# Performance work log

Hardware: AMD Instinct MI355X
Metric: run time of the kernel (lower is better)

The kernel has to match this reference:

```python
import jax, jax.numpy as jnp
import numpy as np

NH = 8        # num_heads
KS = 64       # key_size
C_IN = 256
C_OUT = 3 * NH * KS   # 1536
GROUPS = 3 * NH       # 24
EPS = 1e-5
H = W = 64


def setup_inputs() -> dict:
    key = jax.random.key(0)
    k1, k2 = jax.random.split(key)
    x = jax.random.normal(k1, (1, C_IN, H, W), dtype=jnp.float32)
    conv_w = jax.random.normal(k2, (C_OUT, C_IN, 1, 1), dtype=jnp.float32) * 0.05
    gn_w = jnp.ones((C_OUT,), dtype=jnp.float32)
    gn_b = jnp.zeros((C_OUT,), dtype=jnp.float32)
    return {"x": x, "conv_w": conv_w, "gn_w": gn_w, "gn_b": gn_b}


def reference(x, conv_w, gn_w, gn_b):
    B, _, h, w = x.shape
    # 1x1 conv (normalize=True -> no bias): per-pixel GEMM over channels
    attn = jnp.einsum('bchw,oc->bohw', x, conv_w[:, :, 0, 0])  # [B, 1536, H, W]
    # GroupNorm: 24 groups of KS channels, normalized over (KS, H, W)
    g = attn.reshape(B, GROUPS, -1)
    mean = g.mean(axis=-1, keepdims=True)
    var = g.var(axis=-1, keepdims=True)
    g = (g - mean) * jax.lax.rsqrt(var + EPS)
    attn = g.reshape(B, C_OUT, h, w) * gn_w[None, :, None, None] + gn_b[None, :, None, None]
    # split into key, query, value (in that order, per chunk(3, dim=2))
    attn = attn.reshape(B, NH, 3 * KS, h * w)
    key_, query, value = jnp.split(attn, 3, axis=2)   # each [B, NH, KS, HW]
    # saliency = q^T @ k / sqrt(KS) -> [B, NH, HW, HW]
    saliency = jnp.einsum('bnkq,bnkl->bnql', query, key_) / jnp.sqrt(jnp.float32(KS))
    mask = jax.nn.softmax(saliency, axis=-1)
    # out = v @ mask^T -> [B, NH, KS, HW]
    out = jnp.einsum('bnkl,bnql->bnkq', value, mask)
    return out.reshape(B, NH * KS, h, w)
```

## Files before the change

kernel.cpp:

```cpp
#include <hip/hip_runtime.h>

typedef __bf16 bf16;
typedef __bf16 bf16x8 __attribute__((ext_vector_type(8)));
typedef __bf16 bf16x4 __attribute__((ext_vector_type(4)));
typedef float f32x4 __attribute__((ext_vector_type(4)));
typedef float f32x16 __attribute__((ext_vector_type(16)));


#define QF 0.18033688011112042f
#define EXPF(x) __builtin_amdgcn_exp2f(x)

union U4 { bf16x4 v; unsigned u[2]; };
union U8 { bf16x8 v; unsigned u[4]; };

__global__ void k_misc(const float* __restrict__ x, const float* __restrict__ w,
                       bf16* __restrict__ xT, bf16* __restrict__ wb, float* __restrict__ cs) {
    int b = blockIdx.x;
    if (b < 256) {
        __shared__ float ld[64][65];
        int cb = (b & 3) * 64;
        int pb = (b >> 2) * 64;
        int tp = (threadIdx.x & 15) * 4;
        int tc = threadIdx.x >> 4;
#pragma unroll
        for (int pass = 0; pass < 4; pass++) {
            int c = tc + pass * 16;
            float4 f = *(const float4*)(x + (cb + c) * 4096 + pb + tp);
            ld[tp][c] = f.x; ld[tp + 1][c] = f.y; ld[tp + 2][c] = f.z; ld[tp + 3][c] = f.w;
        }
        __syncthreads();
        int px = threadIdx.x >> 3;
        int co = (threadIdx.x & 7) * 8;
#pragma unroll
        for (int pass = 0; pass < 2; pass++) {
            int p2 = px + pass * 32;
            bf16x8 o;
#pragma unroll
            for (int j = 0; j < 8; j++) o[j] = (bf16)ld[p2][co + j];
            *(bf16x8*)(xT + (pb + p2) * 256 + cb + co) = o;
        }
    } else if (b < 640) {
        int idx = ((b - 256) * 256 + threadIdx.x) * 4;
        float4 f = *(const float4*)(w + idx);
        bf16x4 o;
        o[0] = (bf16)f.x; o[1] = (bf16)f.y; o[2] = (bf16)f.z; o[3] = (bf16)f.w;
        *(bf16x4*)(wb + idx) = o;
    } else {
#pragma unroll
        for (int i = 0; i < 12; i++) cs[i * 256 + threadIdx.x] = 0.f;
    }
}

__global__ __launch_bounds__(256) void k_conv(const bf16* __restrict__ Wb,
                                              const bf16* __restrict__ xT,
                                              bf16* __restrict__ qkvT,
                                              float* __restrict__ cs) {
    __shared__ __attribute__((aligned(16))) bf16 xs[64 * 72];
    __shared__ __attribute__((aligned(16))) bf16 ws2[64 * 72];
    int wid = threadIdx.x >> 6, lane = threadIdx.x & 63;
    int quad = lane >> 4, l15 = lane & 15;
    int g  = blockIdx.x % 24;
    int pb = (blockIdx.x / 24) * 64;
    int h = g / 3, sec = g % 3;
    int ob = g * 64;

    int srow = threadIdx.x >> 2;
    int scol = (threadIdx.x & 3) * 16;

    f32x4 acc[4];
#pragma unroll
    for (int c = 0; c < 4; c++) acc[c] = (f32x4){0.f, 0.f, 0.f, 0.f};

    bf16x8 fx0 = *(const bf16x8*)(xT + (pb + srow) * 256 + scol);
    bf16x8 fx1 = *(const bf16x8*)(xT + (pb + srow) * 256 + scol + 8);
    bf16x8 fw0 = *(const bf16x8*)(Wb + (ob + srow) * 256 + scol);
    bf16x8 fw1 = *(const bf16x8*)(Wb + (ob + srow) * 256 + scol + 8);

    for (int c4 = 0; c4 < 4; c4++) {
        __syncthreads();
        *(bf16x8*)(xs  + srow * 72 + scol)     = fx0;
        *(bf16x8*)(xs  + srow * 72 + scol + 8) = fx1;
        *(bf16x8*)(ws2 + srow * 72 + scol)     = fw0;
        *(bf16x8*)(ws2 + srow * 72 + scol + 8) = fw1;
        __syncthreads();

        if (c4 < 3) {
            int co = (c4 + 1) * 64;
            fx0 = *(const bf16x8*)(xT + (pb + srow) * 256 + co + scol);
            fx1 = *(const bf16x8*)(xT + (pb + srow) * 256 + co + scol + 8);
            fw0 = *(const bf16x8*)(Wb + (ob + srow) * 256 + co + scol);
            fw1 = *(const bf16x8*)(Wb + (ob + srow) * 256 + co + scol + 8);
        }

#pragma unroll
        for (int k2 = 0; k2 < 2; k2++) {
            bf16x8 a = *(const bf16x8*)(ws2 + (wid * 16 + l15) * 72 + k2 * 32 + quad * 8);
#pragma unroll
            for (int c = 0; c < 4; c++) {
                bf16x8 b = *(const bf16x8*)(xs + (c * 16 + l15) * 72 + k2 * 32 + quad * 8);
                acc[c] = __builtin_amdgcn_mfma_f32_16x16x32_bf16(a, b, acc[c], 0, 0, 0);
            }
        }
    }

    int ch0 = wid * 16 + quad * 4;
#pragma unroll
    for (int r = 0; r < 4; r++) {
        float sp  = acc[0][r] + acc[1][r] + acc[2][r] + acc[3][r];
        float ssp = acc[0][r] * acc[0][r] + acc[1][r] * acc[1][r]
                  + acc[2][r] * acc[2][r] + acc[3][r] * acc[3][r];
#pragma unroll
        for (int m = 1; m < 16; m <<= 1) {
            sp  += __shfl_xor(sp,  m, 64);
            ssp += __shfl_xor(ssp, m, 64);
        }
        if (l15 == 0) {
            atomicAdd(cs + (ob + ch0 + r) * 2,     sp);
            atomicAdd(cs + (ob + ch0 + r) * 2 + 1, ssp);
        }
    }

    __syncthreads();
    bf16* tile = xs;
    if (sec == 2) {
#pragma unroll
        for (int c = 0; c < 4; c++)
#pragma unroll
            for (int r = 0; r < 4; r++)
                tile[(ch0 + r) * 72 + c * 16 + l15] = (bf16)acc[c][r];
    } else {
#pragma unroll
        for (int c = 0; c < 4; c++) {
            bf16x4 o;
#pragma unroll
            for (int r = 0; r < 4; r++) o[r] = (bf16)acc[c][r];
            *(bf16x4*)(&tile[(c * 16 + l15) * 72 + ch0]) = o;
        }
    }
    __syncthreads();
    bf16* base = qkvT + h * 786432;
    int t = threadIdx.x;
    if (sec == 2) {
        bf16* V = base + 524288;
#pragma unroll
        for (int it = 0; it < 2; it++) {
            int e = it * 256 + t; int ch = e >> 3; int pxo = (e & 7) * 8;
            *(bf16x8*)(V + ch * 4096 + pb + pxo) = *(const bf16x8*)(&tile[ch * 72 + pxo]);
        }
    } else {
        bf16* dst = base + (sec == 0 ? 262144 : 0);
#pragma unroll
        for (int it = 0; it < 2; it++) {
            int e = it * 256 + t; int px = e >> 3; int cho = (e & 7) * 8;
            *(bf16x8*)(dst + (pb + px) * 64 + cho) = *(const bf16x8*)(&tile[px * 72 + cho]);
        }
    }
}

#define PF_BLOCK(S, PFA, PFB)                                                   \
    {                                                                           \
        float p0 = EXPF(S[0]),  p1 = EXPF(S[1]),  p2 = EXPF(S[2]),  p3 = EXPF(S[3]);   \
        float p4 = EXPF(S[4]),  p5 = EXPF(S[5]),  p6 = EXPF(S[6]),  p7 = EXPF(S[7]);   \
        float p8 = EXPF(S[8]),  p9 = EXPF(S[9]),  p10 = EXPF(S[10]), p11 = EXPF(S[11]); \
        float p12 = EXPF(S[12]), p13 = EXPF(S[13]), p14 = EXPF(S[14]), p15 = EXPF(S[15]); \
        lacc += (((p0 + p1) + (p2 + p3)) + ((p4 + p5) + (p6 + p7)))             \
              + (((p8 + p9) + (p10 + p11)) + ((p12 + p13) + (p14 + p15)));      \
        U4 lo, hi;                                                              \
        lo.v[0] = (bf16)p0;  lo.v[1] = (bf16)p1;  lo.v[2] = (bf16)p2;  lo.v[3] = (bf16)p3;  \
        hi.v[0] = (bf16)p4;  hi.v[1] = (bf16)p5;  hi.v[2] = (bf16)p6;  hi.v[3] = (bf16)p7;  \
        unsigned a0 = lo.u[0], b0 = hi.u[0], a1 = lo.u[1], b1 = hi.u[1];        \
        asm("v_permlane32_swap_b32 %0, %1" : "+v"(a0), "+v"(b0));               \
        asm("v_permlane32_swap_b32 %0, %1" : "+v"(a1), "+v"(b1));               \
        U8 fA; fA.u[0] = a0; fA.u[1] = a1; fA.u[2] = b0; fA.u[3] = b1;          \
        PFA = fA.v;                                                             \
        U4 lo2, hi2;                                                            \
        lo2.v[0] = (bf16)p8;  lo2.v[1] = (bf16)p9;  lo2.v[2] = (bf16)p10; lo2.v[3] = (bf16)p11; \
        hi2.v[0] = (bf16)p12; hi2.v[1] = (bf16)p13; hi2.v[2] = (bf16)p14; hi2.v[3] = (bf16)p15; \
        unsigned a2 = lo2.u[0], b2 = hi2.u[0], a3 = lo2.u[1], b3 = hi2.u[1];    \
        asm("v_permlane32_swap_b32 %0, %1" : "+v"(a2), "+v"(b2));               \
        asm("v_permlane32_swap_b32 %0, %1" : "+v"(a3), "+v"(b3));               \
        U8 fB; fB.u[0] = a2; fB.u[1] = a3; fB.u[2] = b2; fB.u[3] = b3;          \
        PFB = fB.v;                                                             \
    }

#define STAGE(BK, BV)                                                           \
    *(bf16x8*)((BK) + r0 * 72 + koff)        = kf0;                             \
    *(bf16x8*)((BK) + (r0 + 32) * 72 + koff) = kf1;                             \
    *(bf16x8*)((BV) + r0 * 72 + koff)        = vf0;                             \
    *(bf16x8*)((BV) + (r0 + 32) * 72 + koff) = vf1;

#define PREFETCH(T)                                                             \
    {   int nb = (T) * 64;                                                      \
        kf0 = *(const bf16x8*)(KT + (nb + r0) * 64 + koff);                     \
        kf1 = *(const bf16x8*)(KT + (nb + r0 + 32) * 64 + koff);                \
        vf0 = *(const bf16x8*)(V + r0 * 4096 + nb + koff);                      \
        vf1 = *(const bf16x8*)(V + (r0 + 32) * 4096 + nb + koff); }

#define QK_TILE(KSB)                                                            \
    {   const bf16* ka = (KSB) + l31 * 72 + half * 8;                           \
        const bf16* kb = (KSB) + (32 + l31) * 72 + half * 8;                    \
        s0 = (f32x16)(0.0f); s1 = (f32x16)(0.0f);                               \
        __builtin_amdgcn_s_setprio(1);                                          \
        s0 = __builtin_amdgcn_mfma_f32_32x32x16_bf16(*(const bf16x8*)(ka +  0), bq[0], s0, 0, 0, 0); \
        s1 = __builtin_amdgcn_mfma_f32_32x32x16_bf16(*(const bf16x8*)(kb +  0), bq[0], s1, 0, 0, 0); \
        s0 = __builtin_amdgcn_mfma_f32_32x32x16_bf16(*(const bf16x8*)(ka + 16), bq[1], s0, 0, 0, 0); \
        s1 = __builtin_amdgcn_mfma_f32_32x32x16_bf16(*(const bf16x8*)(kb + 16), bq[1], s1, 0, 0, 0); \
        s0 = __builtin_amdgcn_mfma_f32_32x32x16_bf16(*(const bf16x8*)(ka + 32), bq[2], s0, 0, 0, 0); \
        s1 = __builtin_amdgcn_mfma_f32_32x32x16_bf16(*(const bf16x8*)(kb + 32), bq[2], s1, 0, 0, 0); \
        s0 = __builtin_amdgcn_mfma_f32_32x32x16_bf16(*(const bf16x8*)(ka + 48), bq[3], s0, 0, 0, 0); \
        s1 = __builtin_amdgcn_mfma_f32_32x32x16_bf16(*(const bf16x8*)(kb + 48), bq[3], s1, 0, 0, 0); \
        __builtin_amdgcn_s_setprio(0); }

#define PV_TILE(VSB)                                                            \
    {   const bf16* va = (VSB) + l31 * 72 + half * 8;                           \
        const bf16* vb = (VSB) + (32 + l31) * 72 + half * 8;                    \
        __builtin_amdgcn_s_setprio(1);                                          \
        oacc0 = __builtin_amdgcn_mfma_f32_32x32x16_bf16(*(const bf16x8*)(va +  0), pfp0, oacc0, 0, 0, 0); \
        oacc1 = __builtin_amdgcn_mfma_f32_32x32x16_bf16(*(const bf16x8*)(vb +  0), pfp0, oacc1, 0, 0, 0); \
        oacc0 = __builtin_amdgcn_mfma_f32_32x32x16_bf16(*(const bf16x8*)(va + 16), pfp1, oacc0, 0, 0, 0); \
        oacc1 = __builtin_amdgcn_mfma_f32_32x32x16_bf16(*(const bf16x8*)(vb + 16), pfp1, oacc1, 0, 0, 0); \
        oacc0 = __builtin_amdgcn_mfma_f32_32x32x16_bf16(*(const bf16x8*)(va + 32), pfp2, oacc0, 0, 0, 0); \
        oacc1 = __builtin_amdgcn_mfma_f32_32x32x16_bf16(*(const bf16x8*)(vb + 32), pfp2, oacc1, 0, 0, 0); \
        oacc0 = __builtin_amdgcn_mfma_f32_32x32x16_bf16(*(const bf16x8*)(va + 48), pfp3, oacc0, 0, 0, 0); \
        oacc1 = __builtin_amdgcn_mfma_f32_32x32x16_bf16(*(const bf16x8*)(vb + 48), pfp3, oacc1, 0, 0, 0); \
        __builtin_amdgcn_s_setprio(0); }

__global__ __launch_bounds__(256, 3) void k_attn(const bf16* __restrict__ qkvT,
                                                 const float2* __restrict__ cs,
                                                 const float* __restrict__ gnw,
                                                 const float* __restrict__ gnb,
                                                 bf16* __restrict__ Opart,
                                                 float* __restrict__ Lsum) {
    int bid   = blockIdx.x;
    int h     = bid & 7;
    int qb    = (bid >> 3) & 31;
    int split = bid >> 8;
    int wid = threadIdx.x >> 6, lane = threadIdx.x & 63;
    int l31 = lane & 31, half = lane >> 5;
    const bf16* QT = qkvT + h * 786432;
    const bf16* KT = QT + 262144;
    const bf16* V  = QT + 524288;
    int qw = qb * 128 + wid * 32;

    __shared__ __attribute__((aligned(16))) bf16 Ks[2][64 * 72];
    __shared__ __attribute__((aligned(16))) bf16 Vs[2][64 * 72];

    int r0   = threadIdx.x >> 3;
    int koff = (threadIdx.x & 7) * 8;

    float2 vK = cs[(h * 3) * 64 + lane];
    float2 vQ = cs[(h * 3 + 1) * 64 + lane];
    float sK = vK.x, qK = vK.y, sQ = vQ.x, qQ = vQ.y;
#pragma unroll
    for (int m = 1; m < 64; m <<= 1) {
        sK += __shfl_xor(sK, m, 64); qK += __shfl_xor(qK, m, 64);
        sQ += __shfl_xor(sQ, m, 64); qQ += __shfl_xor(qQ, m, 64);
    }
    const float N = 262144.0f;
    float meanK = sK / N, invK = rsqrtf(qK / N - meanK * meanK + 1e-5f);
    float meanQ = sQ / N, invQ = rsqrtf(qQ / N - meanQ * meanQ + 1e-5f);

    bf16x8 bq[4];
#pragma unroll
    for (int ks = 0; ks < 4; ks++) {
        bf16x8 raw = *(const bf16x8*)(QT + (qw + l31) * 64 + ks * 16 + half * 8);
#pragma unroll
        for (int j = 0; j < 8; j++) {
            int c = ks * 16 + half * 8 + j;
            float gwq = gnw[h * 192 + 64 + c] * invQ;
            float qv  = (gwq * (float)raw[j] + (gnb[h * 192 + 64 + c] - meanQ * gwq)) * QF;
            float aKc = gnw[h * 192 + c] * invK;
            bq[ks][j] = (bf16)(aKc * qv);
        }
    }

    f32x16 oacc0 = (f32x16)(0.0f), oacc1 = (f32x16)(0.0f);
    f32x16 s0, s1;
    bf16x8 pfp0, pfp1, pfp2, pfp3;
    float ls = 0.f;

    int t0 = (split * 64) / 3, t1 = ((split + 1) * 64) / 3;

    bf16x8 kf0, kf1, vf0, vf1;
    PREFETCH(t0);

    STAGE(Ks[t0 & 1], Vs[t0 & 1]);
    __syncthreads();
    if (t0 + 1 < t1) PREFETCH(t0 + 1);
    QK_TILE(Ks[t0 & 1]);
    {
        float lacc = ls;
        PF_BLOCK(s0, pfp0, pfp1);
        PF_BLOCK(s1, pfp2, pfp3);
        ls = lacc;
    }

    for (int lt = t0 + 1; lt < t1; lt++) {
        __syncthreads();
        STAGE(Ks[lt & 1], Vs[lt & 1]);
        __syncthreads();
        if (lt + 1 < t1) PREFETCH(lt + 1);
        QK_TILE(Ks[lt & 1]);
        PV_TILE(Vs[(lt - 1) & 1]);
        {
            float lacc = ls;
            PF_BLOCK(s0, pfp0, pfp1);
            PF_BLOCK(s1, pfp2, pfp3);
            ls = lacc;
        }
    }
    PV_TILE(Vs[(t1 - 1) & 1]);

    ls += __shfl_xor(ls, 32, 64);
    if (half == 0)
        Lsum[split * 32768 + h * 4096 + qw + l31] = ls;

    bf16* Ob = Opart + split * 2097152;
#pragma unroll
    for (int r = 0; r < 16; r++) {
        int kd = (r & 3) + 8 * (r >> 2) + 4 * half;
        Ob[(h * 64 + kd) * 4096 + qw + l31]        = (bf16)oacc0[r];
        Ob[(h * 64 + 32 + kd) * 4096 + qw + l31]   = (bf16)oacc1[r];
    }
}

__global__ void k_final(const bf16* __restrict__ Opart, const float* __restrict__ Lsum,
                        const float2* __restrict__ cs, const float* __restrict__ gnw,
                        const float* __restrict__ gnb, float* __restrict__ out) {
    int gid = blockIdx.x * 256 + threadIdx.x;
    int row = gid >> 9;
    int c8  = (gid & 511) << 3;
    int h   = row >> 6;

    int g = h * 3 + 2;
    int c = threadIdx.x & 63;
    float2 v = cs[g * 64 + c];
    float s = v.x, ss = v.y;
#pragma unroll
    for (int m = 1; m < 64; m <<= 1) { s += __shfl_xor(s, m, 64); ss += __shfl_xor(ss, m, 64); }
    const float N = 262144.0f;
    float mean = s / N;
    float inv  = rsqrtf(ss / N - mean * mean + 1e-5f);
    int gi = h * 192 + 128 + (row & 63);
    float gw = gnw[gi];
    float va = inv * gw;
    float vb = gnb[gi] - mean * inv * gw;

    float o[8] = {0, 0, 0, 0, 0, 0, 0, 0};
    float l[8] = {0, 0, 0, 0, 0, 0, 0, 0};
#pragma unroll
    for (int sp = 0; sp < 3; sp++) {
        bf16x8 vv = *(const bf16x8*)(Opart + sp * 2097152 + row * 4096 + c8);
        const float* L = Lsum + sp * 32768 + h * 4096 + c8;
        float4 l0 = *(const float4*)L;
        float4 l1 = *(const float4*)(L + 4);
#pragma unroll
        for (int j = 0; j < 8; j++) o[j] += (float)vv[j];
        l[0] += l0.x; l[1] += l0.y; l[2] += l0.z; l[3] += l0.w;
        l[4] += l1.x; l[5] += l1.y; l[6] += l1.z; l[7] += l1.w;
    }
    float4 r0, r1;
    r0.x = va * o[0] / l[0] + vb; r0.y = va * o[1] / l[1] + vb;
    r0.z = va * o[2] / l[2] + vb; r0.w = va * o[3] / l[3] + vb;
    r1.x = va * o[4] / l[4] + vb; r1.y = va * o[5] / l[5] + vb;
    r1.z = va * o[6] / l[6] + vb; r1.w = va * o[7] / l[7] + vb;
    *(float4*)(out + row * 4096 + c8)     = r0;
    *(float4*)(out + row * 4096 + c8 + 4) = r1;
}

extern "C" void kernel_launch(void* const* d_in, const int* in_sizes, int n_in,
                              void* d_out, int out_size, void* d_ws, size_t ws_size,
                              hipStream_t stream) {
    const float* x      = (const float*)d_in[0];
    const float* conv_w = (const float*)d_in[1];
    const float* gn_w   = (const float*)d_in[2];
    const float* gn_b   = (const float*)d_in[3];
    float* out = (float*)d_out;
    char* ws = (char*)d_ws;

    bf16*   qkvT  = (bf16*) (ws);
    bf16*   Opart = (bf16*) (ws + 12582912);
    bf16*   Wb    = (bf16*) (ws + 12582912);
    bf16*   xT    = (bf16*) (ws + 13369344);
    float*  Lsum  = (float*)(ws + 29360128);
    float*  cs    = (float*)(ws + 29884416);

    hipLaunchKernelGGL(k_misc,  dim3(641),  dim3(256), 0, stream, x, conv_w, xT, Wb, cs);
    hipLaunchKernelGGL(k_conv,  dim3(1536), dim3(256), 0, stream, Wb, xT, qkvT, cs);
    hipLaunchKernelGGL(k_attn,  dim3(768),  dim3(256), 0, stream, qkvT, (const float2*)cs,
                       gn_w, gn_b, Opart, Lsum);
    hipLaunchKernelGGL(k_final, dim3(1024), dim3(256), 0, stream, Opart, Lsum, (const float2*)cs, gn_w, gn_b, out);
}
```

Baseline: 135.8 us.

## Register-block attention over 64 queries per wave and split keys four ways

Each wave now computes a 64-query tile (two 32-row MFMA blocks) instead of 32, so every K/V fragment read from LDS feeds twice as many MFMAs. The key range is split into four equal parts of 16 tiles instead of three uneven parts, with the grid shrunk to 512 blocks and the final reduction extended to four partials. The loop drops the software pipelining that overlapped the previous tile's PV with the current QK, and launch bounds fall to 2 blocks per CU to make room for the doubled accumulators. The intent is to cut LDS traffic per unit of matrix work, at the cost of less latency hiding and lower occupancy.

```diff
diff --git a/kernel.cpp b/kernel.cpp
--- a/kernel.cpp
+++ b/kernel.cpp
@@ -9,6 +9,7 @@
 
 #define QF 0.18033688011112042f
 #define EXPF(x) __builtin_amdgcn_exp2f(x)
+#define MFMA32(A, B, C) __builtin_amdgcn_mfma_f32_32x32x16_bf16(A, B, C, 0, 0, 0)
 
 union U4 { bf16x4 v; unsigned u[2]; };
 union U8 { bf16x8 v; unsigned u[4]; };
@@ -157,13 +158,13 @@
     }
 }
 
-#define PF_BLOCK(S, PFA, PFB)                                                   \
+#define PF_BLOCK(S, LACC, PFA, PFB)                                             \
     {                                                                           \
         float p0 = EXPF(S[0]),  p1 = EXPF(S[1]),  p2 = EXPF(S[2]),  p3 = EXPF(S[3]);   \
         float p4 = EXPF(S[4]),  p5 = EXPF(S[5]),  p6 = EXPF(S[6]),  p7 = EXPF(S[7]);   \
         float p8 = EXPF(S[8]),  p9 = EXPF(S[9]),  p10 = EXPF(S[10]), p11 = EXPF(S[11]); \
         float p12 = EXPF(S[12]), p13 = EXPF(S[13]), p14 = EXPF(S[14]), p15 = EXPF(S[15]); \
-        lacc += (((p0 + p1) + (p2 + p3)) + ((p4 + p5) + (p6 + p7)))             \
+        LACC += (((p0 + p1) + (p2 + p3)) + ((p4 + p5) + (p6 + p7)))             \
               + (((p8 + p9) + (p10 + p11)) + ((p12 + p13) + (p14 + p15)));      \
         U4 lo, hi;                                                              \
         lo.v[0] = (bf16)p0;  lo.v[1] = (bf16)p1;  lo.v[2] = (bf16)p2;  lo.v[3] = (bf16)p3;  \
@@ -196,36 +197,43 @@
         vf0 = *(const bf16x8*)(V + r0 * 4096 + nb + koff);                      \
         vf1 = *(const bf16x8*)(V + (r0 + 32) * 4096 + nb + koff); }
 
-#define QK_TILE(KSB)                                                            \
-    {   const bf16* ka = (KSB) + l31 * 72 + half * 8;                           \
-        const bf16* kb = (KSB) + (32 + l31) * 72 + half * 8;                    \
-        s0 = (f32x16)(0.0f); s1 = (f32x16)(0.0f);                               \
+#define QK64(KSB)                                                               \
+    {   const bf16* kra = (KSB) + l31 * 72 + half * 8;                          \
+        const bf16* krb = (KSB) + (32 + l31) * 72 + half * 8;                   \
         __builtin_amdgcn_s_setprio(1);                                          \
-        s0 = __builtin_amdgcn_mfma_f32_32x32x16_bf16(*(const bf16x8*)(ka +  0), bq[0], s0, 0, 0, 0); \
-        s1 = __builtin_amdgcn_mfma_f32_32x32x16_bf16(*(const bf16x8*)(kb +  0), bq[0], s1, 0, 0, 0); \
-        s0 = __builtin_amdgcn_mfma_f32_32x32x16_bf16(*(const bf16x8*)(ka + 16), bq[1], s0, 0, 0, 0); \
-        s1 = __builtin_amdgcn_mfma_f32_32x32x16_bf16(*(const bf16x8*)(kb + 16), bq[1], s1, 0, 0, 0); \
-        s0 = __builtin_amdgcn_mfma_f32_32x32x16_bf16(*(const bf16x8*)(ka + 32), bq[2], s0, 0, 0, 0); \
-        s1 = __builtin_amdgcn_mfma_f32_32x32x16_bf16(*(const bf16x8*)(kb + 32), bq[2], s1, 0, 0, 0); \
-        s0 = __builtin_amdgcn_mfma_f32_32x32x16_bf16(*(const bf16x8*)(ka + 48), bq[3], s0, 0, 0, 0); \
-        s1 = __builtin_amdgcn_mfma_f32_32x32x16_bf16(*(const bf16x8*)(kb + 48), bq[3], s1, 0, 0, 0); \
+        { bf16x8 fa = *(const bf16x8*)(kra +  0), fb = *(const bf16x8*)(krb +  0); \
+          s00 = MFMA32(fa, bqA[0], s00); s01 = MFMA32(fa, bqB[0], s01);         \
+          s10 = MFMA32(fb, bqA[0], s10); s11 = MFMA32(fb, bqB[0], s11); }       \
+        { bf16x8 fa = *(const bf16x8*)(kra + 16), fb = *(const bf16x8*)(krb + 16); \
+          s00 = MFMA32(fa, bqA[1], s00); s01 = MFMA32(fa, bqB[1], s01);         \
+          s10 = MFMA32(fb, bqA[1], s10); s11 = MFMA32(fb, bqB[1], s11); }       \
+        { bf16x8 fa = *(const bf16x8*)(kra + 32), fb = *(const bf16x8*)(krb + 32); \
+          s00 = MFMA32(fa, bqA[2], s00); s01 = MFMA32(fa, bqB[2], s01);         \
+          s10 = MFMA32(fb, bqA[2], s10); s11 = MFMA32(fb, bqB[2], s11); }       \
+        { bf16x8 fa = *(const bf16x8*)(kra + 48), fb = *(const bf16x8*)(krb + 48); \
+          s00 = MFMA32(fa, bqA[3], s00); s01 = MFMA32(fa, bqB[3], s01);         \
+          s10 = MFMA32(fb, bqA[3], s10); s11 = MFMA32(fb, bqB[3], s11); }       \
         __builtin_amdgcn_s_setprio(0); }
 
-#define PV_TILE(VSB)                                                            \
-    {   const bf16* va = (VSB) + l31 * 72 + half * 8;                           \
-        const bf16* vb = (VSB) + (32 + l31) * 72 + half * 8;                    \
+#define PV64(VSB)                                                               \
+    {   const bf16* vra = (VSB) + l31 * 72 + half * 8;                          \
+        const bf16* vrb = (VSB) + (32 + l31) * 72 + half * 8;                   \
         __builtin_amdgcn_s_setprio(1);                                          \
-        oacc0 = __builtin_amdgcn_mfma_f32_32x32x16_bf16(*(const bf16x8*)(va +  0), pfp0, oacc0, 0, 0, 0); \
-        oacc1 = __builtin_amdgcn_mfma_f32_32x32x16_bf16(*(const bf16x8*)(vb +  0), pfp0, oacc1, 0, 0, 0); \
-        oacc0 = __builtin_amdgcn_mfma_f32_32x32x16_bf16(*(const bf16x8*)(va + 16), pfp1, oacc0, 0, 0, 0); \
-        oacc1 = __builtin_amdgcn_mfma_f32_32x32x16_bf16(*(const bf16x8*)(vb + 16), pfp1, oacc1, 0, 0, 0); \
-        oacc0 = __builtin_amdgcn_mfma_f32_32x32x16_bf16(*(const bf16x8*)(va + 32), pfp2, oacc0, 0, 0, 0); \
-        oacc1 = __builtin_amdgcn_mfma_f32_32x32x16_bf16(*(const bf16x8*)(vb + 32), pfp2, oacc1, 0, 0, 0); \
-        oacc0 = __builtin_amdgcn_mfma_f32_32x32x16_bf16(*(const bf16x8*)(va + 48), pfp3, oacc0, 0, 0, 0); \
-        oacc1 = __builtin_amdgcn_mfma_f32_32x32x16_bf16(*(const bf16x8*)(vb + 48), pfp3, oacc1, 0, 0, 0); \
+        { bf16x8 fa = *(const bf16x8*)(vra +  0), fb = *(const bf16x8*)(vrb +  0); \
+          oA0 = MFMA32(fa, pa0, oA0); oB0 = MFMA32(fa, pb0, oB0);               \
+          oA1 = MFMA32(fb, pa0, oA1); oB1 = MFMA32(fb, pb0, oB1); }             \
+        { bf16x8 fa = *(const bf16x8*)(vra + 16), fb = *(const bf16x8*)(vrb + 16); \
+          oA0 = MFMA32(fa, pa1, oA0); oB0 = MFMA32(fa, pb1, oB0);               \
+          oA1 = MFMA32(fb, pa1, oA1); oB1 = MFMA32(fb, pb1, oB1); }             \
+        { bf16x8 fa = *(const bf16x8*)(vra + 32), fb = *(const bf16x8*)(vrb + 32); \
+          oA0 = MFMA32(fa, pa2, oA0); oB0 = MFMA32(fa, pb2, oB0);               \
+          oA1 = MFMA32(fb, pa2, oA1); oB1 = MFMA32(fb, pb2, oB1); }             \
+        { bf16x8 fa = *(const bf16x8*)(vra + 48), fb = *(const bf16x8*)(vrb + 48); \
+          oA0 = MFMA32(fa, pa3, oA0); oB0 = MFMA32(fa, pb3, oB0);               \
+          oA1 = MFMA32(fb, pa3, oA1); oB1 = MFMA32(fb, pb3, oB1); }             \
         __builtin_amdgcn_s_setprio(0); }
 
-__global__ __launch_bounds__(256, 3) void k_attn(const bf16* __restrict__ qkvT,
+__global__ __launch_bounds__(256, 2) void k_attn(const bf16* __restrict__ qkvT,
                                                  const float2* __restrict__ cs,
                                                  const float* __restrict__ gnw,
                                                  const float* __restrict__ gnb,
@@ -233,14 +241,14 @@
                                                  float* __restrict__ Lsum) {
     int bid   = blockIdx.x;
     int h     = bid & 7;
-    int qb    = (bid >> 3) & 31;
-    int split = bid >> 8;
+    int qb    = (bid >> 3) & 15;
+    int split = bid >> 7;
     int wid = threadIdx.x >> 6, lane = threadIdx.x & 63;
     int l31 = lane & 31, half = lane >> 5;
     const bf16* QT = qkvT + h * 786432;
     const bf16* KT = QT + 262144;
     const bf16* V  = QT + 524288;
-    int qw = qb * 128 + wid * 32;
+    int qw = qb * 256 + wid * 64;
 
     __shared__ __attribute__((aligned(16))) bf16 Ks[2][64 * 72];
     __shared__ __attribute__((aligned(16))) bf16 Vs[2][64 * 72];
@@ -260,67 +268,72 @@
     float meanK = sK / N, invK = rsqrtf(qK / N - meanK * meanK + 1e-5f);
     float meanQ = sQ / N, invQ = rsqrtf(qQ / N - meanQ * meanQ + 1e-5f);
 
-    bf16x8 bq[4];
+    bf16x8 bqA[4], bqB[4];
 #pragma unroll
     for (int ks = 0; ks < 4; ks++) {
-        bf16x8 raw = *(const bf16x8*)(QT + (qw + l31) * 64 + ks * 16 + half * 8);
+        bf16x8 rawA = *(const bf16x8*)(QT + (qw + l31) * 64 + ks * 16 + half * 8);
+        bf16x8 rawB = *(const bf16x8*)(QT + (qw + 32 + l31) * 64 + ks * 16 + half * 8);
 #pragma unroll
         for (int j = 0; j < 8; j++) {
             int c = ks * 16 + half * 8 + j;
             float gwq = gnw[h * 192 + 64 + c] * invQ;
-            float qv  = (gwq * (float)raw[j] + (gnb[h * 192 + 64 + c] - meanQ * gwq)) * QF;
+            float bvq = (gnb[h * 192 + 64 + c] - meanQ * gwq) * QF;
+            float avq = gwq * QF;
             float aKc = gnw[h * 192 + c] * invK;
-            bq[ks][j] = (bf16)(aKc * qv);
-        }
-    }
-
-    f32x16 oacc0 = (f32x16)(0.0f), oacc1 = (f32x16)(0.0f);
-    f32x16 s0, s1;
-    bf16x8 pfp0, pfp1, pfp2, pfp3;
-    float ls = 0.f;
-
-    int t0 = (split * 64) / 3, t1 = ((split + 1) * 64) / 3;
+            bqA[ks][j] = (bf16)(aKc * (avq * (float)rawA[j] + bvq));
+            bqB[ks][j] = (bf16)(aKc * (avq * (float)rawB[j] + bvq));
+        }
+    }
+
+    f32x16 oA0 = (f32x16)(0.0f), oA1 = (f32x16)(0.0f);
+    f32x16 oB0 = (f32x16)(0.0f), oB1 = (f32x16)(0.0f);
+    f32x16 s00, s01, s10, s11;
+    bf16x8 pa0, pa1, pa2, pa3, pb0, pb1, pb2, pb3;
+    float ls0 = 0.f, ls1 = 0.f;
+
+    int t0 = split * 16, t1 = t0 + 16;
 
     bf16x8 kf0, kf1, vf0, vf1;
     PREFETCH(t0);
 
-    STAGE(Ks[t0 & 1], Vs[t0 & 1]);
-    __syncthreads();
-    if (t0 + 1 < t1) PREFETCH(t0 + 1);
-    QK_TILE(Ks[t0 & 1]);
-    {
-        float lacc = ls;
-        PF_BLOCK(s0, pfp0, pfp1);
-        PF_BLOCK(s1, pfp2, pfp3);
-        ls = lacc;
-    }
-
-    for (int lt = t0 + 1; lt < t1; lt++) {
-        __syncthreads();
-        STAGE(Ks[lt & 1], Vs[lt & 1]);
+    for (int lt = t0; lt < t1; lt++) {
+        bf16* ksb = Ks[lt & 1];
+        bf16* vsb = Vs[lt & 1];
+        STAGE(ksb, vsb);
         __syncthreads();
         if (lt + 1 < t1) PREFETCH(lt + 1);
-        QK_TILE(Ks[lt & 1]);
-        PV_TILE(Vs[(lt - 1) & 1]);
+
+        s00 = (f32x16)(0.0f); s01 = (f32x16)(0.0f);
+        s10 = (f32x16)(0.0f); s11 = (f32x16)(0.0f);
+        QK64(ksb);
+
         {
-            float lacc = ls;
-            PF_BLOCK(s0, pfp0, pfp1);
-            PF_BLOCK(s1, pfp2, pfp3);
-            ls = lacc;
-        }
-    }
-    PV_TILE(Vs[(t1 - 1) & 1]);
-
-    ls += __shfl_xor(ls, 32, 64);
-    if (half == 0)
-        Lsum[split * 32768 + h * 4096 + qw + l31] = ls;
+            float la0 = ls0, la1 = ls1;
+            PF_BLOCK(s00, la0, pa0, pa1);
+            PF_BLOCK(s10, la0, pa2, pa3);
+            PF_BLOCK(s01, la1, pb0, pb1);
+            PF_BLOCK(s11, la1, pb2, pb3);
+            ls0 = la0; ls1 = la1;
+        }
+
+        PV64(vsb);
+    }
+
+    ls0 += __shfl_xor(ls0, 32, 64);
+    ls1 += __shfl_xor(ls1, 32, 64);
+    if (half == 0) {
+        Lsum[split * 32768 + h * 4096 + qw + l31]      = ls0;
+        Lsum[split * 32768 + h * 4096 + qw + 32 + l31] = ls1;
+    }
 
     bf16* Ob = Opart + split * 2097152;
 #pragma unroll
     for (int r = 0; r < 16; r++) {
         int kd = (r & 3) + 8 * (r >> 2) + 4 * half;
-        Ob[(h * 64 + kd) * 4096 + qw + l31]        = (bf16)oacc0[r];
-        Ob[(h * 64 + 32 + kd) * 4096 + qw + l31]   = (bf16)oacc1[r];
+        Ob[(h * 64 + kd) * 4096 + qw + l31]           = (bf16)oA0[r];
+        Ob[(h * 64 + 32 + kd) * 4096 + qw + l31]      = (bf16)oA1[r];
+        Ob[(h * 64 + kd) * 4096 + qw + 32 + l31]      = (bf16)oB0[r];
+        Ob[(h * 64 + 32 + kd) * 4096 + qw + 32 + l31] = (bf16)oB1[r];
     }
 }
 
@@ -349,7 +362,7 @@
     float o[8] = {0, 0, 0, 0, 0, 0, 0, 0};
     float l[8] = {0, 0, 0, 0, 0, 0, 0, 0};
 #pragma unroll
-    for (int sp = 0; sp < 3; sp++) {
+    for (int sp = 0; sp < 4; sp++) {
         bf16x8 vv = *(const bf16x8*)(Opart + sp * 2097152 + row * 4096 + c8);
         const float* L = Lsum + sp * 32768 + h * 4096 + c8;
         float4 l0 = *(const float4*)L;
@@ -387,7 +400,7 @@
 
     hipLaunchKernelGGL(k_misc,  dim3(641),  dim3(256), 0, stream, x, conv_w, xT, Wb, cs);
     hipLaunchKernelGGL(k_conv,  dim3(1536), dim3(256), 0, stream, Wb, xT, qkvT, cs);
-    hipLaunchKernelGGL(k_attn,  dim3(768),  dim3(256), 0, stream, qkvT, (const float2*)cs,
+    hipLaunchKernelGGL(k_attn,  dim3(512),  dim3(256), 0, stream, qkvT, (const float2*)cs,
                        gn_w, gn_b, Opart, Lsum);
     hipLaunchKernelGGL(k_final, dim3(1024), dim3(256), 0, stream, Opart, Lsum, (const float2*)cs, gn_w, gn_b, out);
 }
```

Result: faster. 130.8 us (-3.7%).
